# Performance work log

Hardware: AMD Instinct MI355X
Metric: run time of the kernel (lower is better)

Reference implementation:

```python
import jax, jax.numpy as jnp
import numpy as np

B, S, H, NL, DF, VF = 8, 2048, 8, 128, 64, 64
NF, HS = 1280, 33
FEAT = NF + HS
NLAYERS = 2
MAXLAP = 0.001


def setup_inputs() -> dict:
    key = jax.random.key(0)
    ks = jax.random.split(key, 11)
    u = lambda k, shape: jax.random.uniform(k, shape, jnp.float32, -0.01, 0.01)
    return {
        "latent_outputs": jax.random.normal(ks[0], (B, S, HS), jnp.float32),
        "masks": (jax.random.uniform(ks[1], (B, S, 1)) > 0.05).astype(jnp.float32),
        "x_embeds": jax.random.normal(ks[2], (B, S, NF), jnp.float32),
        "pos_embed": jax.random.normal(ks[3], (B, S, DF), jnp.float32),
        "collect_classes": u(ks[4], (1, VF * H, HS)),
        "query_linear": u(ks[5], (NLAYERS, 1, H, FEAT + 1, DF)),
        "key_linear": u(ks[6], (NLAYERS, 1, 1, FEAT + 1, DF)),
        "value_linear": u(ks[7], (NLAYERS, 1, H, FEAT + 1, VF)),
        "project_original": u(ks[8], (NLAYERS, 1, 1, FEAT + 1, VF)),
        "aggregation_params": u(ks[9], (NLAYERS, 1, H, 1, 1)),
        "collect_feats": u(ks[10], (NLAYERS - 1, VF * H, FEAT)),
    }


def _iterative_inv(mat, n_iter=6):
    I = jnp.eye(mat.shape[-1], dtype=mat.dtype)
    key = mat
    value = (1.0 / jnp.max(jnp.sum(key, axis=-2))) * jnp.swapaxes(key, -1, -2)
    for _ in range(n_iter):
        kv = key @ value
        value = 0.25 * value @ (13 * I - kv @ (15 * I - kv @ (7 * I - kv)))
    return value


def _compute_accum(values, masks, qw, kw, vw, agg):
    # values: [B,1,S,FEAT]; qw/vw: [1,H,FEAT+1,*], kw: [1,1,FEAT+1,DF]
    # NOTE: bias is the second-to-last row (as in the torch source, [..., -2:-1, :]).
    Eq = values @ qw[..., :-1, :] + qw[..., -2:-1, :]  # [B,H,S,DF]
    Ek = values @ kw[..., :-1, :] + kw[..., -2:-1, :]  # [B,1,S,DF]
    Ev = values @ vw[..., :-1, :] + vw[..., -2:-1, :]  # [B,H,S,VF]
    pos = jnp.arange(S)
    rel = jnp.abs(pos[None, None, None, :] - pos[None, None, :, None]).astype(values.dtype)
    sigmas = jnp.abs(agg) + MAXLAP          # [1,H,1,1]
    pos_mask = -sigmas * rel                # [1,H,S,S] Laplace position penalty
    scale = DF ** 0.25
    Eq = Eq / scale
    Ek = Ek / scale
    seg = S // NL
    q_land = Eq.reshape(Eq.shape[0], Eq.shape[1], NL, seg, DF).mean(-2)  # [B,H,NL,DF]
    k_land = Ek.reshape(Ek.shape[0], Ek.shape[1], NL, seg, DF).mean(-2)  # [B,1,NL,DF]
    pos_sel = pos_mask.reshape(1, H, NL, seg, S).mean(3)                 # [1,H,NL,S]
    kernel_1 = jax.nn.softmax(Eq @ jnp.swapaxes(k_land, -1, -2)
                              + jnp.swapaxes(pos_sel, -1, -2), axis=-1)  # [B,H,S,NL]
    pos_sel2 = pos_sel.reshape(1, H, NL, NL, seg).mean(-1)               # [1,H,NL,NL]
    kernel_2 = jax.nn.softmax(q_land @ jnp.swapaxes(k_land, -1, -2) + pos_sel2, axis=-1)
    scores = q_land @ jnp.swapaxes(Ek, -1, -2)                            # [B,H,NL,S]
    attn_mask = jnp.swapaxes(jnp.where(masks[:, None] == 0, -1e6, 0.0), -1, -2)  # [B,1,1,S]
    kernel_3 = jax.nn.softmax(scores + attn_mask + pos_sel, axis=-1)      # [B,H,NL,S]
    probs = kernel_1 @ _iterative_inv(kernel_2)                           # [B,H,S,NL]
    return probs @ (kernel_3 @ Ev)                                        # [B,H,S,VF]


def reference(latent_outputs, masks, x_embeds, pos_embed, collect_classes,
              query_linear, key_linear, value_linear, project_original,
              aggregation_params, collect_feats):
    cl = jax.nn.softmax(latent_outputs, axis=-1) * masks
    orig = jnp.concatenate([x_embeds, cl], axis=-1)[:, None]  # [B,1,S,FEAT]
    va = orig
    for layer in range(NLAYERS):
        va = _compute_accum(va, masks, query_linear[layer], key_linear[layer],
                            value_linear[layer], aggregation_params[layer])
        pw = project_original[layer, ..., :-1, :]
        pb = project_original[layer, ..., -2:-1, :]
        va = va + (orig @ pw + pb) / NLAYERS            # [B,H,S,VF]
        va = jnp.transpose(va, (0, 2, 1, 3)).reshape(B, S, H * VF)
        cw = collect_feats[layer] if layer < NLAYERS - 1 else collect_classes
        va = (va @ cw)[:, None]
    return va[:, 0] * masks  # [B,S,HS]
```

## Files before the change

### kernel.cpp

```cpp
#include <hip/hip_runtime.h>
#include <math.h>


namespace {

constexpr int B = 8, S = 2048, H = 8, NL = 128, DF = 64, VF = 64;
constexpr int NF = 1280, HS = 33, FEAT = 1313, FEATP = 1314;
constexpr int SEG = 16, HV = H * VF;
constexpr int KSF = 1344;
constexpr int NSPL = 4;
constexpr long ROWS = (long)B * S;
constexpr float INV_SCALE = 0.35355339059327373f;

typedef _Float16 f16;
typedef _Float16 f16x8 __attribute__((ext_vector_type(8)));
typedef _Float16 f16x4 __attribute__((ext_vector_type(4)));
typedef float f32x4 __attribute__((ext_vector_type(4)));

__global__ __launch_bounds__(256) void k_cl(
    const float* __restrict__ lat, const float* __restrict__ masks,
    float* __restrict__ cl)
{
  long row = (long)blockIdx.x * 4 + (threadIdx.x >> 6);
  int l = threadIdx.x & 63;
  float v = (l < HS) ? lat[row * HS + l] : -INFINITY;
  float m = v;
  #pragma unroll
  for (int o = 32; o; o >>= 1) m = fmaxf(m, __shfl_xor(m, o));
  float e = (l < HS) ? expf(v - m) : 0.f;
  float s = e;
  #pragma unroll
  for (int o = 32; o; o >>= 1) s += __shfl_xor(s, o);
  if (l < HS) cl[row * HS + l] = e / s * masks[row];
}

__global__ __launch_bounds__(256) void k_cvta(
    const float* __restrict__ xemb, const float* __restrict__ cl,
    f16* __restrict__ dst)
{
  long idx = (long)blockIdx.x * 256 + threadIdx.x;
  long row = idx / 168;
  int c = (int)(idx - row * 168);
  int t = c >> 3, cs = c & 7;
  int k0 = t * 64 + cs * 8;
  f16x8 v;
  if (t < 20) {
    float4 a = *(const float4*)&xemb[row * NF + k0];
    float4 b = *(const float4*)&xemb[row * NF + k0 + 4];
    v[0] = (f16)a.x; v[1] = (f16)a.y; v[2] = (f16)a.z; v[3] = (f16)a.w;
    v[4] = (f16)b.x; v[5] = (f16)b.y; v[6] = (f16)b.z; v[7] = (f16)b.w;
  } else {
    #pragma unroll
    for (int i = 0; i < 8; ++i) {
      int k = k0 + i;
      float f = 0.f;
      if (k < NF) f = xemb[row * NF + k];
      else if (k < FEAT) f = cl[row * HS + (k - NF)];
      v[i] = (f16)f;
    }
  }
  int cd = cs ^ ((int)row & 7);
  *(f16x8*)&dst[row * KSF + t * 64 + cd * 8] = v;
}

__global__ __launch_bounds__(256) void k_cvtw6(
    const float* __restrict__ qlin, const float* __restrict__ klin,
    const float* __restrict__ vlin, const float* __restrict__ plin,
    const float* __restrict__ cfeat, const float* __restrict__ ccls,
    f16* __restrict__ WQt, f16* __restrict__ WKt, f16* __restrict__ WVt,
    f16* __restrict__ WPt, f16* __restrict__ WCFt, f16* __restrict__ WCCt)
{
  constexpr long s1 = 172032, s2 = 193536, s3 = 365568, s4 = 387072,
                 s5 = 473088, s6 = 477184;
  long idx = (long)blockIdx.x * 256 + threadIdx.x;
  if (idx >= s6) return;
  const float* src; f16* dst; int K, N, Npad, KS; long srcZ, rel;
  if (idx < s1)      { src = qlin;  dst = WQt;  K = FEAT; N = 64;  Npad = 64;  KS = KSF; srcZ = (long)FEATP * 64; rel = idx; }
  else if (idx < s2) { src = klin;  dst = WKt;  K = FEAT; N = 64;  Npad = 64;  KS = KSF; srcZ = (long)FEATP * 64; rel = idx - s1; }
  else if (idx < s3) { src = vlin;  dst = WVt;  K = FEAT; N = 64;  Npad = 64;  KS = KSF; srcZ = (long)FEATP * 64; rel = idx - s2; }
  else if (idx < s4) { src = plin;  dst = WPt;  K = FEAT; N = 64;  Npad = 64;  KS = KSF; srcZ = (long)FEATP * 64; rel = idx - s3; }
  else if (idx < s5) { src = cfeat; dst = WCFt; K = 512;  N = FEAT; Npad = KSF; KS = 512; srcZ = 0; rel = idx - s4; }
  else               { src = ccls;  dst = WCCt; K = 512;  N = HS;  Npad = 64;  KS = 512; srcZ = 0; rel = idx - s5; }
  long cpz = (long)Npad * (KS >> 3);
  long z = rel / cpz;
  long rem = rel - z * cpz;
  int n = (int)(rem / (KS >> 3));
  int c = (int)(rem - (long)n * (KS >> 3));
  int t = c >> 3, cs = c & 7;
  int cd = cs ^ (n & 7);
  int k0 = t * 64 + cd * 8;
  const float* sp = src + z * srcZ;
  f16x8 v;
  #pragma unroll
  for (int i = 0; i < 8; ++i) {
    int k = k0 + i;
    v[i] = (f16)((k < K && n < N) ? sp[(long)k * N + n] : 0.f);
  }
  *(f16x8*)&dst[rel * 8] = v;
}

__global__ __launch_bounds__(256, 2) void k_mgemm(
    const f16* __restrict__ A, long aZOff, int aDiv,
    const f16* __restrict__ Wt, long wZOff, int wMod,
    int KT, int mode,
    float* __restrict__ C, long cZOff, int ldC,
    const float* __restrict__ biasBase, long biasZOff, float scale,
    f16* __restrict__ outA, int NR, const float* __restrict__ mask)
{
  const long KS = (long)KT * 64;
  int z = blockIdx.z;
  const f16* Ap = A + (long)(z / aDiv) * aZOff;
  const f16* Wp = Wt + (long)(z % wMod) * wZOff;
  long m0 = (long)blockIdx.x * 256;
  int n0 = blockIdx.y * 64;
  constexpr int BOFF = 256 * 64;
  __shared__ f16 lds[2][(256 + 64) * 64];
  int tid = threadIdx.x;
  int wv = tid >> 6, l = tid & 63;

  const f16* aW = Ap + (m0 + wv * 64 + (l >> 3)) * KS + (l & 7) * 8;
  const f16* bW = Wp + ((long)(n0 + wv * 16 + (l >> 3))) * KS + (l & 7) * 8;

  f32x4 acc[4][4];
  #pragma unroll
  for (int i = 0; i < 4; ++i)
    #pragma unroll
    for (int j = 0; j < 4; ++j) acc[i][j] = (f32x4){0.f, 0.f, 0.f, 0.f};

  auto stage = [&](int buf, int t) {
    f16* la = &lds[buf][(wv * 64) * 64];
    const f16* ga = aW + (long)t * 64;
// ... 69 lines not shown
      int coll = ni * 16 + lcn;
      int col = n0 + coll;
      bool ok = col < NR;
      #pragma unroll
      for (int mi = 0; mi < 4; ++mi) {
        int rowl = wv * 64 + mi * 16 + lr;
        #pragma unroll
        for (int r = 0; r < 4; ++r) {
          float v = ok ? acc[mi][ni][r] * scale : 0.f;
          st[(rowl + r) * 64 + coll] = (f16)v;
        }
      }
    }
    __syncthreads();
    int tt = n0 >> 6;
    for (int c = tid; c < 2048; c += 256) {
      int row = c >> 3, cd = c & 7;
      long grow = m0 + row;
      int r7 = (int)grow & 7;
      f16x8 v = *(const f16x8*)&st[row * 64 + cd * 8];
      *(f16x8*)&outA[grow * KSF + tt * 64 + ((cd ^ r7) << 3)] = v;
    }
  }
}

__global__ __launch_bounds__(256, 2) void k_qve(
    const f16* __restrict__ Aact, const f16* __restrict__ Aorig,
    const f16* __restrict__ WQl, const f16* __restrict__ WVl,
    const f16* __restrict__ wk, const f16* __restrict__ wp,
    const float* __restrict__ bqBase, const float* __restrict__ bvBase,
    const float* __restrict__ bk, const float* __restrict__ bp,
    f16* __restrict__ Eq16, f16* __restrict__ Ev16, f16* __restrict__ Ek16,
    float* __restrict__ projb,
    float* __restrict__ qland, f16* __restrict__ qland16,
    float* __restrict__ kland, f16* __restrict__ kland16)
{
  constexpr int KT = 21;
  __shared__ __align__(16) f16 shbuf[2 * 256 * 64];
  int bid = blockIdx.x;
  int tid = threadIdx.x;
  int wv = tid >> 6, l = tid & 63;
  int l15 = l & 15, lc = l >> 4, lx = l & 7;
  int lr = (l >> 4) * 4;
  int lcn = l & 15;

  if (bid < 1024) {
    constexpr int BOFF = 128 * 64;
    int z = bid >> 4;
    int h = z & 7;
    const f16* Ap = Aact + (long)(z >> 3) * S * KSF;
    const f16* wqp = WQl + (long)h * 64 * KSF;
    const f16* wvp = WVl + (long)h * 64 * KSF;
    const float* bq = bqBase + (long)h * FEATP * 64;
    const float* bv = bvBase + (long)h * FEATP * 64;
    long m0 = (long)(bid & 15) * 128;

    const f16* aW = Ap + (m0 + wv * 32 + (l >> 3)) * KSF + (l & 7) * 8;

    f32x4 acc[2][8];
    #pragma unroll
    for (int i = 0; i < 2; ++i)
      #pragma unroll
      for (int j = 0; j < 8; ++j) acc[i][j] = (f32x4){0.f, 0.f, 0.f, 0.f};

    auto stage = [&](int buf, int t) {
      f16* la = &shbuf[buf * 16384 + (wv * 32) * 64];
      const f16* ga = aW + (long)t * 64;
      #pragma unroll
// ... 47 lines not shown
        }
      __syncthreads();
    }

    f16* st = &shbuf[0];
    #pragma unroll
    for (int ni = 0; ni < 8; ++ni) {
      int col = ni * 16 + l15;
      float bvv = (col < 64) ? bq[col] : bv[col - 64];
      float scl = (col < 64) ? INV_SCALE : 1.f;
      #pragma unroll
      for (int mi = 0; mi < 2; ++mi) {
        int rowl = wv * 32 + mi * 16 + lr;
        #pragma unroll
        for (int r = 0; r < 4; ++r)
          st[(rowl + r) * 128 + col] = (f16)((acc[mi][ni][r] + bvv) * scl);
      }
    }
    __syncthreads();
    f16* oq = Eq16 + (long)z * S * 64;
    f16* ov = Ev16 + (long)z * S * 64;
    for (int c = tid; c < 1024; c += 256) {
      int rw = c >> 3, cc = c & 7;
      *(f16x8*)&oq[(m0 + rw) * 64 + cc * 8] = *(const f16x8*)&st[rw * 128 + cc * 8];
      *(f16x8*)&ov[(m0 + rw) * 64 + cc * 8] = *(const f16x8*)&st[rw * 128 + 64 + cc * 8];
    }
    for (int c = tid; c < 512; c += 256) {
      int lm = c >> 6, d = c & 63;
      float s = 0.f;
      #pragma unroll
      for (int i = 0; i < SEG; ++i) s += (float)st[(lm * SEG + i) * 128 + d];
      float v = s * (1.f / SEG);
      long li = (long)z * NL + (m0 >> 4) + lm;
      qland[li * 64 + d] = v;
      qland16[li * 64 + d] = (f16)v;
    }
  } else {
    constexpr int BOFF = 128 * 64;
    int rel = bid - 1024;
    int zz2 = rel >> 4;
    int prob = zz2 >> 3, b = zz2 & 7;
    const f16* Ap = (prob ? Aorig : Aact) + (long)b * S * KSF;
    const f16* Wp = prob ? wp : wk;
    long m0 = (long)(rel & 15) * 128;

    const f16* aW = Ap + (m0 + wv * 32 + (l >> 3)) * KSF + (l & 7) * 8;
    const f16* bW = Wp + ((long)(wv * 16 + (l >> 3))) * KSF + (l & 7) * 8;

    f32x4 acc[2][4];
    #pragma unroll
    for (int i = 0; i < 2; ++i)
      #pragma unroll
      for (int j = 0; j < 4; ++j) acc[i][j] = (f32x4){0.f, 0.f, 0.f, 0.f};

    auto stage = [&](int buf, int t) {
      f16* la = &shbuf[buf * 12288 + (wv * 32) * 64];
      const f16* ga = aW + (long)t * 64;
      #pragma unroll
      for (int j = 0; j < 4; ++j)
        __builtin_amdgcn_global_load_lds(
            (const __attribute__((address_space(1))) void*)(ga + (long)j * 8 * KSF),
            (__attribute__((address_space(3))) void*)(la + j * 512), 16, 0, 0);
      f16* lb = &shbuf[buf * 12288 + BOFF + (wv * 16) * 64];
      const f16* gb = bW + (long)t * 64;
      #pragma unroll
      for (int j = 0; j < 2; ++j)
        __builtin_amdgcn_global_load_lds(
// ... 31 lines not shown
          acc[mi][ni] = __builtin_amdgcn_mfma_f32_16x16x32_f16(af[mi][1], bf[ni][1], acc[mi][ni], 0, 0, 0);
        }
      __syncthreads();
    }

    if (prob == 0) {
      f16* st = &shbuf[0];
      #pragma unroll
      for (int ni = 0; ni < 4; ++ni) {
        int col = ni * 16 + lcn;
        float bv = bk[col];
        #pragma unroll
        for (int mi = 0; mi < 2; ++mi) {
          int rowl = wv * 32 + mi * 16 + lr;
          #pragma unroll
          for (int r = 0; r < 4; ++r)
            st[(rowl + r) * 64 + col] = (f16)((acc[mi][ni][r] + bv) * INV_SCALE);
        }
      }
      __syncthreads();
      f16* o16 = Ek16 + (long)b * S * 64;
      for (int c = tid; c < 1024; c += 256) {
        int row = c >> 3, cc = c & 7;
        f16x8 v = *(const f16x8*)&st[row * 64 + cc * 8];
        *(f16x8*)&o16[(m0 + row) * 64 + cc * 8] = v;
      }
      for (int c = tid; c < 512; c += 256) {
        int lm = c >> 6, d = c & 63;
        float s = 0.f;
        #pragma unroll
        for (int i = 0; i < SEG; ++i) s += (float)st[(lm * SEG + i) * 64 + d];
        float v = s * (1.f / SEG);
        long li = (long)b * NL + (m0 >> 4) + lm;
        kland[li * 64 + d] = v;
        kland16[li * 64 + d] = (f16)v;
      }
    } else {
      float* Cp = projb + (long)b * S * 64;
      #pragma unroll
      for (int ni = 0; ni < 4; ++ni) {
        int col = ni * 16 + lcn;
        float bv = bp[col];
        #pragma unroll
        for (int mi = 0; mi < 2; ++mi) {
          long row = m0 + wv * 32 + mi * 16 + lr;
          #pragma unroll
          for (int r = 0; r < 4; ++r)
            Cp[(row + r) * 64 + col] = (acc[mi][ni][r] + bv) * 0.5f;
        }
      }
    }
  }
}

__global__ __launch_bounds__(256) void k_kernel2(
    const float* __restrict__ qland, const float* __restrict__ kland,
    const float* __restrict__ aggL, f16* __restrict__ k2h,
    float* __restrict__ colmax)
{
  int z = blockIdx.x; int b = z / H; int h = z % H;
  float sigma = fabsf(aggL[h]) + 0.001f;
  __shared__ float qs[NL][68];
  __shared__ float ks[NL][68];
  __shared__ float lg[NL][NL + 1];
  int tid = threadIdx.x;
  for (int idx = tid; idx < NL * DF; idx += 256) {
    int r = idx >> 6, d = idx & 63;
    qs[r][d] = qland[((long)z * NL + r) * DF + d];
    ks[r][d] = kland[((long)b * NL + r) * DF + d];
  }
  __syncthreads();
  int r = tid >> 1, half = tid & 1;
  float lmax = -INFINITY;
  for (int c = 0; c < 64; c++) {
    int m = half * 64 + c;
    float s = 0.f;
    #pragma unroll
    for (int d = 0; d < DF; d += 4) {
      float4 q = *(const float4*)&qs[r][d];
      float4 k4 = *(const float4*)&ks[m][d];
      s += q.x * k4.x + q.y * k4.y + q.z * k4.z + q.w * k4.w;
    }
    float dd = fabsf((float)(r - m));
    s += -sigma * ((r == m) ? 5.3125f : 16.f * dd);
    lg[r][m] = s;
    lmax = fmaxf(lmax, s);
  }
  lmax = fmaxf(lmax, __shfl_xor(lmax, 1));
  float lsum = 0.f;
  for (int c = 0; c < 64; c++) {
    int m = half * 64 + c;
    float e = expf(lg[r][m] - lmax);
    lg[r][m] = e; lsum += e;
  }
  lsum += __shfl_xor(lsum, 1);
  float inv = 1.f / lsum;
  for (int c = 0; c < 64; c++) {
    int m = half * 64 + c;
    float p = lg[r][m] * inv;
    lg[r][m] = p;
    k2h[((long)z * NL + r) * NL + m] = (f16)p;
  }
  __syncthreads();
  float myc = 0.f;
  if (tid < NL) {
    for (int rr = 0; rr < NL; rr++) myc += lg[rr][tid];
  }
  float wm = myc;
  #pragma unroll
  for (int o = 32; o; o >>= 1) wm = fmaxf(wm, __shfl_xor(wm, o));
  __shared__ float wred[4];
  if ((tid & 63) == 0) wred[tid >> 6] = wm;
  __syncthreads();
  if (tid == 0)
    colmax[z] = fmaxf(fmaxf(wred[0], wred[1]), fmaxf(wred[2], wred[3]));
}

__global__ __launch_bounds__(256, 2) void k_kernel3(
    const f16* __restrict__ qland16, const f16* __restrict__ Ek16,
    const f16* __restrict__ Ev16, const float* __restrict__ aggL,
    const float* __restrict__ masks,
    float* __restrict__ partU, float* __restrict__ partML)
{
  __shared__ __align__(16) f16 Qs[64 * 64];
  __shared__ __align__(16) f16 Ks[128 * 64];
  __shared__ __align__(16) f16 Vt[64 * 128];
  __shared__ __align__(16) f16 Pb[4 * 16 * 128];
  __shared__ float Ms[128];
  int id = blockIdx.x;
  int chunk = id & (NSPL - 1);
  int z2 = id >> 2;
  int z = z2 >> 1, half = z2 & 1;
  int b = z >> 3, h = z & 7;
  int q0 = half * 64;
  int tid = threadIdx.x;
  int w = tid >> 6, l = tid & 63;
  float sigma = fabsf(aggL[h]) + 0.001f;
  float cpos = -sigma * (1.f / 16.f);

  for (int c = tid; c < 64 * 8; c += 256) {
    int q = c >> 3, kc = c & 7;
    f16x8 v = *(const f16x8*)&qland16[((long)z * NL + q0 + q) * 64 + kc * 8];
    *(f16x8*)&Qs[q * 64 + ((kc ^ (q & 7)) << 3)] = v;
  }

  f16* Pw = &Pb[w * 16 * 128];
  int l15 = l & 15, lg4 = l >> 4, l7 = l & 7;
  f32x4 Oa[4];
  #pragma unroll
  for (int i = 0; i < 4; ++i) Oa[i] = (f32x4){0.f, 0.f, 0.f, 0.f};
  float mrun[4] = {-INFINITY, -INFINITY, -INFINITY, -INFINITY};
  float lrun[4] = {0.f, 0.f, 0.f, 0.f};

  int t0beg = chunk * (S / 128 / NSPL), t0end = t0beg + S / 128 / NSPL;
  for (int t0 = t0beg; t0 < t0end; ++t0) {
    __syncthreads();
    for (int c = tid; c < 1024; c += 256) {
      int k = c >> 3, kc = c & 7;
      f16x8 v = *(const f16x8*)&Ek16[((long)b * S + t0 * 128 + k) * 64 + kc * 8];
      *(f16x8*)&Ks[k * 64 + ((kc ^ (k & 7)) << 3)] = v;
    }
    for (int c = tid; c < 1024; c += 256) {
      int k = c & 127, dc = c >> 7;
      f16x8 v = *(const f16x8*)&Ev16[((long)z * S + t0 * 128 + k) * 64 + dc * 8];
      int kc = k >> 3, ki = k & 7;
      #pragma unroll
      for (int j = 0; j < 8; ++j) {
        int d = dc * 8 + j;
        Vt[d * 128 + ((kc ^ (d & 7)) << 3) + ki] = v[j];
      }
    }
    if (tid < 128)
      Ms[tid] = (masks[(long)b * S + t0 * 128 + tid] == 0.f) ? -1e6f : 0.f;
    __syncthreads();

    f16x8 af[2];
    #pragma unroll
    for (int kh = 0; kh < 2; ++kh)
      af[kh] = *(const f16x8*)&Qs[(w * 16 + l15) * 64 + (((kh * 4 + lg4) ^ l7) << 3)];
    f32x4 sc[8];
    #pragma unroll
    for (int ct = 0; ct < 8; ++ct) {
      int n = ct * 16 + l15;
      f16x8 b0 = *(const f16x8*)&Ks[n * 64 + (((lg4) ^ (n & 7)) << 3)];
      f16x8 b1 = *(const f16x8*)&Ks[n * 64 + (((4 + lg4) ^ (n & 7)) << 3)];
      f32x4 zz = (f32x4){0.f, 0.f, 0.f, 0.f};
      zz = __builtin_amdgcn_mfma_f32_16x16x32_f16(af[0], b0, zz, 0, 0, 0);
      sc[ct] = __builtin_amdgcn_mfma_f32_16x16x32_f16(af[1], b1, zz, 0, 0, 0);
    }
    float tmax[4] = {-INFINITY, -INFINITY, -INFINITY, -INFINITY};
    #pragma unroll
    for (int ct = 0; ct < 8; ++ct) {
      float mk = Ms[ct * 16 + l15];
      int key = t0 * 128 + ct * 16 + l15;
      #pragma unroll
      for (int r = 0; r < 4; ++r) {
        int qg = q0 + w * 16 + lg4 * 4 + r;
        float a = (float)(key - 16 * qg);
        float ac = fminf(fmaxf(a, 0.f), 15.f);
        float dd = fabsf(a - ac);
        float sum = ac * ac - 15.f * ac + 120.f + 16.f * dd;
        float s = sc[ct][r] + cpos * sum + mk;
        sc[ct][r] = s;
        tmax[r] = fmaxf(tmax[r], s);
      }
    }
    #pragma unroll
    for (int r = 0; r < 4; ++r) {
      #pragma unroll
      for (int o = 1; o < 16; o <<= 1)
        tmax[r] = fmaxf(tmax[r], __shfl_xor(tmax[r], o));
    }
    float fr[4], lsum[4];
    #pragma unroll
    for (int r = 0; r < 4; ++r) {
      float mnew = fmaxf(mrun[r], tmax[r]);
      fr[r] = expf(mrun[r] - mnew);
      mrun[r] = mnew;
      lsum[r] = 0.f;
    }
    #pragma unroll
    for (int ct = 0; ct < 8; ++ct) {
      #pragma unroll
      for (int r = 0; r < 4; ++r) {
        float p = expf(sc[ct][r] - mrun[r]);
        sc[ct][r] = p;
        lsum[r] += p;
      }
    }
    #pragma unroll
    for (int r = 0; r < 4; ++r) {
      #pragma unroll
      for (int o = 1; o < 16; o <<= 1)
        lsum[r] += __shfl_xor(lsum[r], o);
      lrun[r] = lrun[r] * fr[r] + lsum[r];
    }
    f32x4 fv = (f32x4){fr[0], fr[1], fr[2], fr[3]};
    #pragma unroll
    for (int dt = 0; dt < 4; ++dt) Oa[dt] *= fv;
    #pragma unroll
    for (int ct = 0; ct < 8; ++ct) {
      int kc = ct * 2 + (l15 >> 3);
      int ki = l15 & 7;
      #pragma unroll
      for (int r = 0; r < 4; ++r) {
        int row = lg4 * 4 + r;
        Pw[row * 128 + ((kc ^ (row & 7)) << 3) + ki] = (f16)sc[ct][r];
      }
    }
    #pragma unroll
    for (int ks = 0; ks < 4; ++ks) {
      f16x8 pa = *(const f16x8*)&Pw[l15 * 128 + (((ks * 4 + lg4) ^ l7) << 3)];
      #pragma unroll
      for (int dt = 0; dt < 4; ++dt) {
        int n = dt * 16 + l15;
        f16x8 bv = *(const f16x8*)&Vt[n * 128 + (((ks * 4 + lg4) ^ (n & 7)) << 3)];
        Oa[dt] = __builtin_amdgcn_mfma_f32_16x16x32_f16(pa, bv, Oa[dt], 0, 0, 0);
      }
    }
  }
  #pragma unroll
  for (int r = 0; r < 4; ++r) {
    long qg = q0 + w * 16 + lg4 * 4 + r;
    long base = ((long)z * NL + qg) * NSPL + chunk;
    #pragma unroll
    for (int dt = 0; dt < 4; ++dt)
      partU[base * 64 + dt * 16 + l15] = Oa[dt][r];
    if (l15 == 0) {
      partML[base * 2] = mrun[r];
      partML[base * 2 + 1] = lrun[r];
    }
  }
}

__global__ __launch_bounds__(512) void k_inverse(
    const f16* __restrict__ k2h, const float* __restrict__ colmax,
    const float* __restrict__ partU, const float* __restrict__ partML,
    float* __restrict__ m2)
{
  __shared__ __align__(16) f16 bufA[128 * 128];
  __shared__ __align__(16) f16 bufB[128 * 128];
  __shared__ __align__(16) f16 Vt[128 * 128];
  __shared__ __align__(16) f16 Pt[128 * 128];
  int z = blockIdx.x;
  int tid = threadIdx.x;
  int w = tid >> 6, l = tid & 63;
  int l15 = l & 15, lg4 = l >> 4;
  int wr = (w >> 1) * 32, wc = (w & 1) * 64;

  float cv = colmax[l];
  #pragma unroll
  for (int o = 32; o; o >>= 1) cv = fmaxf(cv, __shfl_xor(cv, o));
  float recip = 1.f / cv;

  const f16* key = k2h + (long)z * NL * NL;
  auto swz = [](int r, int c) { return r * 128 + ((((c >> 3) ^ (r & 15))) << 3) + (c & 7); };

  for (int idx = tid; idx < 128 * 16; idx += 512) {
    int r = idx >> 4, c8 = (idx & 15) << 3;
    f16x8 kk = *(const f16x8*)&key[r * 128 + c8];
    f16x8 sv;
    #pragma unroll
    for (int j = 0; j < 8; ++j) sv[j] = (f16)(recip * (float)kk[j]);
    *(f16x8*)&Vt[swz(r, c8)] = sv;
// ... 248 lines not shown
  const float* masks = (const float*)d_in[1];
  const float* xemb  = (const float*)d_in[2];
  const float* ccls  = (const float*)d_in[4];
  const float* qlin  = (const float*)d_in[5];
  const float* klin  = (const float*)d_in[6];
  const float* vlin  = (const float*)d_in[7];
  const float* plin  = (const float*)d_in[8];
  const float* agg   = (const float*)d_in[9];
  const float* cfeat = (const float*)d_in[10];
  float* out = (float*)d_out;
  float* ws = (float*)d_ws;

  long off = 0;
  auto allocF = [&](long n) { float* p = ws + off; off += (n + 3) & ~3L; return p; };
  auto allocH = [&](long n) { f16* p = (f16*)(ws + off); off += ((n + 1) / 2 + 3) & ~3L; return p; };

  f16* origA = allocH(ROWS * KSF);
  f16* vbufA = allocH(ROWS * KSF);
  f16* merged = allocH(ROWS * (long)HV);
  f16* WQt = allocH(16L * 64 * KSF);
  f16* WKt = allocH(2L * 64 * KSF);
  f16* WVt = allocH(16L * 64 * KSF);
  f16* WPt = allocH(2L * 64 * KSF);
  f16* WCFt = allocH((long)KSF * 512);
  f16* WCCt = allocH(64L * 512);
  f16* Ek16 = allocH((long)B * S * 64);
  f16* Ev16 = allocH((long)B * H * S * 64);
  f16* Eq16 = allocH((long)B * H * S * 64);
  f16* qland16 = allocH((long)B * H * NL * DF);
  f16* kland16 = allocH((long)B * NL * DF);
  f16* k2h = allocH((long)B * H * NL * NL);
  float* cl     = allocF(ROWS * HS);
  float* projb  = allocF((long)B * S * VF);
  float* qland  = allocF((long)B * H * NL * DF);
  float* kland  = allocF((long)B * NL * DF);
  float* m2b    = allocF((long)B * H * NL * VF);
  float* colmax = allocF(64);
  float* partU  = allocF((long)B * H * NL * NSPL * 64);
  float* partML = allocF((long)B * H * NL * NSPL * 2);

  k_cl<<<(int)(ROWS / 4), 256, 0, stream>>>(lat, masks, cl);
  k_cvta<<<(int)(ROWS * 168 / 256), 256, 0, stream>>>(xemb, cl, origA);
  k_cvtw6<<<1864, 256, 0, stream>>>(qlin, klin, vlin, plin, cfeat, ccls,
      WQt, WKt, WVt, WPt, WCFt, WCCt);

  const f16* Aact = origA;
  for (int layer = 0; layer < 2; ++layer) {
    const f16* wq = WQt + (long)layer * 8 * 64 * KSF;
    const f16* wk = WKt + (long)layer * 64 * KSF;
    const f16* wvv = WVt + (long)layer * 8 * 64 * KSF;
    const f16* wp = WPt + (long)layer * 64 * KSF;
    const float* bq = qlin + (long)layer * 8 * FEATP * 64 + (long)(FEATP - 2) * 64;
    const float* bk = klin + (long)layer * FEATP * 64 + (long)(FEATP - 2) * 64;
    const float* bv = vlin + (long)layer * 8 * FEATP * 64 + (long)(FEATP - 2) * 64;
    const float* bp = plin + (long)layer * FEATP * 64 + (long)(FEATP - 2) * 64;
    const float* ag = agg + layer * H;

    k_qve<<<1280, 256, 0, stream>>>(Aact, origA, wq, wvv, wk, wp,
        bq, bv, bk, bp, Eq16, Ev16, Ek16, projb,
        qland, qland16, kland, kland16);

    k_kernel2<<<B * H, 256, 0, stream>>>(qland, kland, ag, k2h, colmax);
    k_kernel3<<<B * H * 2 * NSPL, 256, 0, stream>>>(qland16, Ek16, Ev16, ag, masks,
        partU, partML);
    k_inverse<<<B * H, 512, 0, stream>>>(k2h, colmax, partU, partML, m2b);
    k_k1attn<<<B * H * (S / 64), 256, 0, stream>>>(Eq16, kland16, ag, m2b, projb, merged);

    if (layer == 0) {
      dim3 gC(64, 21, 1);
      k_mgemm<<<gC, 256, 0, stream>>>(merged, 0, 1, WCFt, 0, 1, 8, 1,
          nullptr, 0, 0, nullptr, 0, 1.0f, vbufA, FEAT, nullptr);
      Aact = vbufA;
    } else {
      dim3 gO(64, 1, 1);
      k_mgemm<<<gO, 256, 0, stream>>>(merged, 0, 1, WCCt, 0, 1, 8, 2,
          out, 0, HS, nullptr, 0, 1.0f, nullptr, HS, masks);
    }
  }
  (void)in_sizes; (void)n_in; (void)out_size; (void)ws_size;
}
```

Before: 492.4 us.

## Merge prep kernels and fuse landmark kernel2/kernel3 into one MFMA launch

Merges the activation and weight fp16 conversion kernels into a single launch, and merges the landmark-softmax (kernel_2) and landmark-to-sequence attention (kernel_3) kernels into one launch split by block index. The kernel_2 path now uses fp16 MFMA on the fp16 landmark copies instead of fp32 scalar dot products, so the fp32 landmark buffers and their stores are removed. This cuts launch count and lets the small 64-block kernel_2 run concurrently with kernel_3. In exchange, kernel_2 scores are computed from fp16 inputs, which lowers precision ahead of the iterative inverse.

```diff
diff --git a/kernel.cpp b/kernel.cpp
--- a/kernel.cpp
+++ b/kernel.cpp
@@ -34,69 +34,70 @@
   if (l < HS) cl[row * HS + l] = e / s * masks[row];
 }
 
-__global__ __launch_bounds__(256) void k_cvta(
+__global__ __launch_bounds__(256) void k_prep(
     const float* __restrict__ xemb, const float* __restrict__ cl,
-    f16* __restrict__ dst)
-{
-  long idx = (long)blockIdx.x * 256 + threadIdx.x;
-  long row = idx / 168;
-  int c = (int)(idx - row * 168);
-  int t = c >> 3, cs = c & 7;
-  int k0 = t * 64 + cs * 8;
-  f16x8 v;
-  if (t < 20) {
-    float4 a = *(const float4*)&xemb[row * NF + k0];
-    float4 b = *(const float4*)&xemb[row * NF + k0 + 4];
-    v[0] = (f16)a.x; v[1] = (f16)a.y; v[2] = (f16)a.z; v[3] = (f16)a.w;
-    v[4] = (f16)b.x; v[5] = (f16)b.y; v[6] = (f16)b.z; v[7] = (f16)b.w;
-  } else {
-    #pragma unroll
-    for (int i = 0; i < 8; ++i) {
-      int k = k0 + i;
-      float f = 0.f;
-      if (k < NF) f = xemb[row * NF + k];
-      else if (k < FEAT) f = cl[row * HS + (k - NF)];
-      v[i] = (f16)f;
-    }
-  }
-  int cd = cs ^ ((int)row & 7);
-  *(f16x8*)&dst[row * KSF + t * 64 + cd * 8] = v;
-}
-
-__global__ __launch_bounds__(256) void k_cvtw6(
     const float* __restrict__ qlin, const float* __restrict__ klin,
     const float* __restrict__ vlin, const float* __restrict__ plin,
     const float* __restrict__ cfeat, const float* __restrict__ ccls,
+    f16* __restrict__ origA,
     f16* __restrict__ WQt, f16* __restrict__ WKt, f16* __restrict__ WVt,
     f16* __restrict__ WPt, f16* __restrict__ WCFt, f16* __restrict__ WCCt)
 {
-  constexpr long s1 = 172032, s2 = 193536, s3 = 365568, s4 = 387072,
-                 s5 = 473088, s6 = 477184;
-  long idx = (long)blockIdx.x * 256 + threadIdx.x;
-  if (idx >= s6) return;
-  const float* src; f16* dst; int K, N, Npad, KS; long srcZ, rel;
-  if (idx < s1)      { src = qlin;  dst = WQt;  K = FEAT; N = 64;  Npad = 64;  KS = KSF; srcZ = (long)FEATP * 64; rel = idx; }
-  else if (idx < s2) { src = klin;  dst = WKt;  K = FEAT; N = 64;  Npad = 64;  KS = KSF; srcZ = (long)FEATP * 64; rel = idx - s1; }
-  else if (idx < s3) { src = vlin;  dst = WVt;  K = FEAT; N = 64;  Npad = 64;  KS = KSF; srcZ = (long)FEATP * 64; rel = idx - s2; }
-  else if (idx < s4) { src = plin;  dst = WPt;  K = FEAT; N = 64;  Npad = 64;  KS = KSF; srcZ = (long)FEATP * 64; rel = idx - s3; }
-  else if (idx < s5) { src = cfeat; dst = WCFt; K = 512;  N = FEAT; Npad = KSF; KS = 512; srcZ = 0; rel = idx - s4; }
-  else               { src = ccls;  dst = WCCt; K = 512;  N = HS;  Npad = 64;  KS = 512; srcZ = 0; rel = idx - s5; }
-  long cpz = (long)Npad * (KS >> 3);
-  long z = rel / cpz;
-  long rem = rel - z * cpz;
-  int n = (int)(rem / (KS >> 3));
-  int c = (int)(rem - (long)n * (KS >> 3));
-  int t = c >> 3, cs = c & 7;
-  int cd = cs ^ (n & 7);
-  int k0 = t * 64 + cd * 8;
-  const float* sp = src + z * srcZ;
-  f16x8 v;
-  #pragma unroll
-  for (int i = 0; i < 8; ++i) {
-    int k = k0 + i;
-    v[i] = (f16)((k < K && n < N) ? sp[(long)k * N + n] : 0.f);
-  }
-  *(f16x8*)&dst[rel * 8] = v;
+  long bid = blockIdx.x;
+  int tid = threadIdx.x;
+  if (bid < 10752) {
+    long idx = bid * 256 + tid;
+    long row = idx / 168;
+    int c = (int)(idx - row * 168);
+    int t = c >> 3, cs = c & 7;
+    int k0 = t * 64 + cs * 8;
+    f16x8 v;
+    if (t < 20) {
+      float4 a = *(const float4*)&xemb[row * NF + k0];
+      float4 b = *(const float4*)&xemb[row * NF + k0 + 4];
+      v[0] = (f16)a.x; v[1] = (f16)a.y; v[2] = (f16)a.z; v[3] = (f16)a.w;
+      v[4] = (f16)b.x; v[5] = (f16)b.y; v[6] = (f16)b.z; v[7] = (f16)b.w;
+    } else {
+      #pragma unroll
+      for (int i = 0; i < 8; ++i) {
+        int k = k0 + i;
+        float f = 0.f;
+        if (k < NF) f = xemb[row * NF + k];
+        else if (k < FEAT) f = cl[row * HS + (k - NF)];
+        v[i] = (f16)f;
+      }
+    }
+    int cd = cs ^ ((int)row & 7);
+    *(f16x8*)&origA[row * KSF + t * 64 + cd * 8] = v;
+  } else {
+    constexpr long s1 = 172032, s2 = 193536, s3 = 365568, s4 = 387072,
+                   s5 = 473088, s6 = 477184;
+    long idx = (bid - 10752) * 256 + tid;
+    if (idx >= s6) return;
+    const float* src; f16* dst; int K, N, Npad, KS; long srcZ, rel;
+    if (idx < s1)      { src = qlin;  dst = WQt;  K = FEAT; N = 64;  Npad = 64;  KS = KSF; srcZ = (long)FEATP * 64; rel = idx; }
+    else if (idx < s2) { src = klin;  dst = WKt;  K = FEAT; N = 64;  Npad = 64;  KS = KSF; srcZ = (long)FEATP * 64; rel = idx - s1; }
+    else if (idx < s3) { src = vlin;  dst = WVt;  K = FEAT; N = 64;  Npad = 64;  KS = KSF; srcZ = (long)FEATP * 64; rel = idx - s2; }
+    else if (idx < s4) { src = plin;  dst = WPt;  K = FEAT; N = 64;  Npad = 64;  KS = KSF; srcZ = (long)FEATP * 64; rel = idx - s3; }
+    else if (idx < s5) { src = cfeat; dst = WCFt; K = 512;  N = FEAT; Npad = KSF; KS = 512; srcZ = 0; rel = idx - s4; }
+    else               { src = ccls;  dst = WCCt; K = 512;  N = HS;  Npad = 64;  KS = 512; srcZ = 0; rel = idx - s5; }
+    long cpz = (long)Npad * (KS >> 3);
+    long z = rel / cpz;
+    long rem = rel - z * cpz;
+    int n = (int)(rem / (KS >> 3));
+    int c = (int)(rem - (long)n * (KS >> 3));
+    int t = c >> 3, cs = c & 7;
+    int cd = cs ^ (n & 7);
+    int k0 = t * 64 + cd * 8;
+    const float* sp = src + z * srcZ;
+    f16x8 v;
+    #pragma unroll
+    for (int i = 0; i < 8; ++i) {
+      int k = k0 + i;
+      v[i] = (f16)((k < K && n < N) ? sp[(long)k * N + n] : 0.f);
+    }
+    *(f16x8*)&dst[rel * 8] = v;
+  }
 }
 
 __global__ __launch_bounds__(256, 2) void k_mgemm(
@@ -232,8 +233,7 @@
     const float* __restrict__ bk, const float* __restrict__ bp,
     f16* __restrict__ Eq16, f16* __restrict__ Ev16, f16* __restrict__ Ek16,
     float* __restrict__ projb,
-    float* __restrict__ qland, f16* __restrict__ qland16,
-    float* __restrict__ kland, f16* __restrict__ kland16)
+    f16* __restrict__ qland16, f16* __restrict__ kland16)
 {
   constexpr int KT = 21;
   __shared__ __align__(16) f16 shbuf[2 * 256 * 64];
@@ -347,7 +347,6 @@
       for (int i = 0; i < SEG; ++i) s += (float)st[(lm * SEG + i) * 128 + d];
       float v = s * (1.f / SEG);
       long li = (long)z * NL + (m0 >> 4) + lm;
-      qland[li * 64 + d] = v;
       qland16[li * 64 + d] = (f16)v;
     }
   } else {
@@ -445,7 +444,6 @@
         for (int i = 0; i < SEG; ++i) s += (float)st[(lm * SEG + i) * 64 + d];
         float v = s * (1.f / SEG);
         long li = (long)b * NL + (m0 >> 4) + lm;
-        kland[li * 64 + d] = v;
         kland16[li * 64 + d] = (f16)v;
       }
     } else {
@@ -466,223 +464,274 @@
   }
 }
 
-__global__ __launch_bounds__(256) void k_kernel2(
-    const float* __restrict__ qland, const float* __restrict__ kland,
-    const float* __restrict__ aggL, f16* __restrict__ k2h,
-    float* __restrict__ colmax)
+__global__ __launch_bounds__(256, 2) void k_land(
+    const f16* __restrict__ qland16, const f16* __restrict__ kland16,
+    const f16* __restrict__ Ek16, const f16* __restrict__ Ev16,
+    const float* __restrict__ aggL, const float* __restrict__ masks,
+    float* __restrict__ partU, float* __restrict__ partML,
+    f16* __restrict__ k2h, float* __restrict__ colmax)
 {
-  int z = blockIdx.x; int b = z / H; int h = z % H;
-  float sigma = fabsf(aggL[h]) + 0.001f;
-  __shared__ float qs[NL][68];
-  __shared__ float ks[NL][68];
-  __shared__ float lg[NL][NL + 1];
-  int tid = threadIdx.x;
-  for (int idx = tid; idx < NL * DF; idx += 256) {
-    int r = idx >> 6, d = idx & 63;
-    qs[r][d] = qland[((long)z * NL + r) * DF + d];
-    ks[r][d] = kland[((long)b * NL + r) * DF + d];
-  }
-  __syncthreads();
-  int r = tid >> 1, half = tid & 1;
-  float lmax = -INFINITY;
-  for (int c = 0; c < 64; c++) {
-    int m = half * 64 + c;
-    float s = 0.f;
-    #pragma unroll
-    for (int d = 0; d < DF; d += 4) {
-      float4 q = *(const float4*)&qs[r][d];
-      float4 k4 = *(const float4*)&ks[m][d];
-      s += q.x * k4.x + q.y * k4.y + q.z * k4.z + q.w * k4.w;
-    }
-    float dd = fabsf((float)(r - m));
-    s += -sigma * ((r == m) ? 5.3125f : 16.f * dd);
-    lg[r][m] = s;
-    lmax = fmaxf(lmax, s);
-  }
-  lmax = fmaxf(lmax, __shfl_xor(lmax, 1));
-  float lsum = 0.f;
-  for (int c = 0; c < 64; c++) {
-    int m = half * 64 + c;
-    float e = expf(lg[r][m] - lmax);
-    lg[r][m] = e; lsum += e;
-  }
-  lsum += __shfl_xor(lsum, 1);
-  float inv = 1.f / lsum;
-  for (int c = 0; c < 64; c++) {
-    int m = half * 64 + c;
-    float p = lg[r][m] * inv;
-    lg[r][m] = p;
-    k2h[((long)z * NL + r) * NL + m] = (f16)p;
-  }
-  __syncthreads();
-  float myc = 0.f;
-  if (tid < NL) {
-    for (int rr = 0; rr < NL; rr++) myc += lg[rr][tid];
-  }
-  float wm = myc;
-  #pragma unroll
-  for (int o = 32; o; o >>= 1) wm = fmaxf(wm, __shfl_xor(wm, o));
-  __shared__ float wred[4];
-  if ((tid & 63) == 0) wred[tid >> 6] = wm;
-  __syncthreads();
-  if (tid == 0)
-    colmax[z] = fmaxf(fmaxf(wred[0], wred[1]), fmaxf(wred[2], wred[3]));
-}
-
-__global__ __launch_bounds__(256, 2) void k_kernel3(
-    const f16* __restrict__ qland16, const f16* __restrict__ Ek16,
-    const f16* __restrict__ Ev16, const float* __restrict__ aggL,
-    const float* __restrict__ masks,
-    float* __restrict__ partU, float* __restrict__ partML)
-{
-  __shared__ __align__(16) f16 Qs[64 * 64];
-  __shared__ __align__(16) f16 Ks[128 * 64];
-  __shared__ __align__(16) f16 Vt[64 * 128];
-  __shared__ __align__(16) f16 Pb[4 * 16 * 128];
-  __shared__ float Ms[128];
-  int id = blockIdx.x;
-  int chunk = id & (NSPL - 1);
-  int z2 = id >> 2;
-  int z = z2 >> 1, half = z2 & 1;
-  int b = z >> 3, h = z & 7;
-  int q0 = half * 64;
+  __shared__ __align__(16) unsigned char smem[57856];
+  int bid = blockIdx.x;
   int tid = threadIdx.x;
   int w = tid >> 6, l = tid & 63;
-  float sigma = fabsf(aggL[h]) + 0.001f;
-  float cpos = -sigma * (1.f / 16.f);
-
-  for (int c = tid; c < 64 * 8; c += 256) {
-    int q = c >> 3, kc = c & 7;
-    f16x8 v = *(const f16x8*)&qland16[((long)z * NL + q0 + q) * 64 + kc * 8];
-    *(f16x8*)&Qs[q * 64 + ((kc ^ (q & 7)) << 3)] = v;
-  }
-
-  f16* Pw = &Pb[w * 16 * 128];
   int l15 = l & 15, lg4 = l >> 4, l7 = l & 7;
-  f32x4 Oa[4];
-  #pragma unroll
-  for (int i = 0; i < 4; ++i) Oa[i] = (f32x4){0.f, 0.f, 0.f, 0.f};
-  float mrun[4] = {-INFINITY, -INFINITY, -INFINITY, -INFINITY};
-  float lrun[4] = {0.f, 0.f, 0.f, 0.f};
-
-  int t0beg = chunk * (S / 128 / NSPL), t0end = t0beg + S / 128 / NSPL;
-  for (int t0 = t0beg; t0 < t0end; ++t0) {
+
+  if (bid < 512) {
+    f16* Qs = (f16*)smem;
+    f16* Ks = (f16*)(smem + 8192);
+    f16* Vt = (f16*)(smem + 24576);
+    f16* Pb = (f16*)(smem + 40960);
+    float* Ms = (float*)(smem + 57344);
+    int chunk = bid & (NSPL - 1);
+    int z2 = bid >> 2;
+    int z = z2 >> 1, half = z2 & 1;
+    int b = z >> 3, h = z & 7;
+    int q0 = half * 64;
+    float sigma = fabsf(aggL[h]) + 0.001f;
+    float cpos = -sigma * (1.f / 16.f);
+
+    for (int c = tid; c < 64 * 8; c += 256) {
+      int q = c >> 3, kc = c & 7;
+      f16x8 v = *(const f16x8*)&qland16[((long)z * NL + q0 + q) * 64 + kc * 8];
+      *(f16x8*)&Qs[q * 64 + ((kc ^ (q & 7)) << 3)] = v;
+    }
+
+    f16* Pw = &Pb[w * 16 * 128];
+    f32x4 Oa[4];
+    #pragma unroll
+    for (int i = 0; i < 4; ++i) Oa[i] = (f32x4){0.f, 0.f, 0.f, 0.f};
+    float mrun[4] = {-INFINITY, -INFINITY, -INFINITY, -INFINITY};
+    float lrun[4] = {0.f, 0.f, 0.f, 0.f};
+
+    int t0beg = chunk * (S / 128 / NSPL), t0end = t0beg + S / 128 / NSPL;
+    for (int t0 = t0beg; t0 < t0end; ++t0) {
+      __syncthreads();
+      for (int c = tid; c < 1024; c += 256) {
+        int k = c >> 3, kc = c & 7;
+        f16x8 v = *(const f16x8*)&Ek16[((long)b * S + t0 * 128 + k) * 64 + kc * 8];
+        *(f16x8*)&Ks[k * 64 + ((kc ^ (k & 7)) << 3)] = v;
+      }
+      for (int c = tid; c < 1024; c += 256) {
+        int k = c & 127, dc = c >> 7;
+        f16x8 v = *(const f16x8*)&Ev16[((long)z * S + t0 * 128 + k) * 64 + dc * 8];
+        int kc = k >> 3, ki = k & 7;
+        #pragma unroll
+        for (int j = 0; j < 8; ++j) {
+          int d = dc * 8 + j;
+          Vt[d * 128 + ((kc ^ (d & 7)) << 3) + ki] = v[j];
+        }
+      }
+      if (tid < 128)
+        Ms[tid] = (masks[(long)b * S + t0 * 128 + tid] == 0.f) ? -1e6f : 0.f;
+      __syncthreads();
+
+      f16x8 af[2];
+      #pragma unroll
+      for (int kh = 0; kh < 2; ++kh)
+        af[kh] = *(const f16x8*)&Qs[(w * 16 + l15) * 64 + (((kh * 4 + lg4) ^ l7) << 3)];
+      f32x4 sc[8];
+      #pragma unroll
+      for (int ct = 0; ct < 8; ++ct) {
+        int n = ct * 16 + l15;
+        f16x8 b0 = *(const f16x8*)&Ks[n * 64 + (((lg4) ^ (n & 7)) << 3)];
+        f16x8 b1 = *(const f16x8*)&Ks[n * 64 + (((4 + lg4) ^ (n & 7)) << 3)];
+        f32x4 zz = (f32x4){0.f, 0.f, 0.f, 0.f};
+        zz = __builtin_amdgcn_mfma_f32_16x16x32_f16(af[0], b0, zz, 0, 0, 0);
+        sc[ct] = __builtin_amdgcn_mfma_f32_16x16x32_f16(af[1], b1, zz, 0, 0, 0);
+      }
+      float tmax[4] = {-INFINITY, -INFINITY, -INFINITY, -INFINITY};
+      #pragma unroll
+      for (int ct = 0; ct < 8; ++ct) {
+        float mk = Ms[ct * 16 + l15];
+        int key = t0 * 128 + ct * 16 + l15;
+        #pragma unroll
+        for (int r = 0; r < 4; ++r) {
+          int qg = q0 + w * 16 + lg4 * 4 + r;
+          float a = (float)(key - 16 * qg);
+          float ac = fminf(fmaxf(a, 0.f), 15.f);
+          float dd = fabsf(a - ac);
+          float sum = ac * ac - 15.f * ac + 120.f + 16.f * dd;
+          float s = sc[ct][r] + cpos * sum + mk;
+          sc[ct][r] = s;
+          tmax[r] = fmaxf(tmax[r], s);
+        }
+      }
+      #pragma unroll
+      for (int r = 0; r < 4; ++r) {
+        #pragma unroll
+        for (int o = 1; o < 16; o <<= 1)
+          tmax[r] = fmaxf(tmax[r], __shfl_xor(tmax[r], o));
+      }
+      float fr[4], lsum[4];
+      #pragma unroll
+      for (int r = 0; r < 4; ++r) {
+        float mnew = fmaxf(mrun[r], tmax[r]);
+        fr[r] = expf(mrun[r] - mnew);
+        mrun[r] = mnew;
+        lsum[r] = 0.f;
+      }
+      #pragma unroll
+      for (int ct = 0; ct < 8; ++ct) {
+        #pragma unroll
+        for (int r = 0; r < 4; ++r) {
+          float p = expf(sc[ct][r] - mrun[r]);
+          sc[ct][r] = p;
+          lsum[r] += p;
+        }
+      }
+      #pragma unroll
+      for (int r = 0; r < 4; ++r) {
+        #pragma unroll
+        for (int o = 1; o < 16; o <<= 1)
+          lsum[r] += __shfl_xor(lsum[r], o);
+        lrun[r] = lrun[r] * fr[r] + lsum[r];
+      }
+      f32x4 fv = (f32x4){fr[0], fr[1], fr[2], fr[3]};
+      #pragma unroll
+      for (int dt = 0; dt < 4; ++dt) Oa[dt] *= fv;
+      #pragma unroll
+      for (int ct = 0; ct < 8; ++ct) {
+        int kc = ct * 2 + (l15 >> 3);
+        int ki = l15 & 7;
+        #pragma unroll
+        for (int r = 0; r < 4; ++r) {
+          int row = lg4 * 4 + r;
+          Pw[row * 128 + ((kc ^ (row & 7)) << 3) + ki] = (f16)sc[ct][r];
+        }
+      }
+      #pragma unroll
+      for (int ks = 0; ks < 4; ++ks) {
+        f16x8 pa = *(const f16x8*)&Pw[l15 * 128 + (((ks * 4 + lg4) ^ l7) << 3)];
+        #pragma unroll
+        for (int dt = 0; dt < 4; ++dt) {
+          int n = dt * 16 + l15;
+          f16x8 bv = *(const f16x8*)&Vt[n * 128 + (((ks * 4 + lg4) ^ (n & 7)) << 3)];
+          Oa[dt] = __builtin_amdgcn_mfma_f32_16x16x32_f16(pa, bv, Oa[dt], 0, 0, 0);
+        }
+      }
+    }
+    #pragma unroll
+    for (int r = 0; r < 4; ++r) {
+      long qg = q0 + w * 16 + lg4 * 4 + r;
+      long base = ((long)z * NL + qg) * NSPL + chunk;
+      #pragma unroll
+      for (int dt = 0; dt < 4; ++dt)
+        partU[base * 64 + dt * 16 + l15] = Oa[dt][r];
+      if (l15 == 0) {
+        partML[base * 2] = mrun[r];
+        partML[base * 2 + 1] = lrun[r];
+      }
+    }
+  } else {
+    f16* Qs2 = (f16*)smem;
+    f16* Ks2 = (f16*)(smem + 16384);
+    float* colpart = (float*)(smem + 32768);
+    int z = bid - 512;
+    int b2 = z >> 3, h2 = z & 7;
+    float sigma = fabsf(aggL[h2]) + 0.001f;
+    for (int c = tid; c < 1024; c += 256) {
+      int q = c >> 3, kc = c & 7;
+      f16x8 v = *(const f16x8*)&qland16[((long)z * NL + q) * 64 + kc * 8];
+      *(f16x8*)&Qs2[q * 64 + ((kc ^ (q & 7)) << 3)] = v;
+      f16x8 u = *(const f16x8*)&kland16[((long)b2 * NL + q) * 64 + kc * 8];
+      *(f16x8*)&Ks2[q * 64 + ((kc ^ (q & 7)) << 3)] = u;
+    }
     __syncthreads();
-    for (int c = tid; c < 1024; c += 256) {
-      int k = c >> 3, kc = c & 7;
-      f16x8 v = *(const f16x8*)&Ek16[((long)b * S + t0 * 128 + k) * 64 + kc * 8];
-      *(f16x8*)&Ks[k * 64 + ((kc ^ (k & 7)) << 3)] = v;
-    }
-    for (int c = tid; c < 1024; c += 256) {
-      int k = c & 127, dc = c >> 7;
-      f16x8 v = *(const f16x8*)&Ev16[((long)z * S + t0 * 128 + k) * 64 + dc * 8];
-      int kc = k >> 3, ki = k & 7;
-      #pragma unroll
-      for (int j = 0; j < 8; ++j) {
-        int d = dc * 8 + j;
-        Vt[d * 128 + ((kc ^ (d & 7)) << 3) + ki] = v[j];
-      }
-    }
-    if (tid < 128)
-      Ms[tid] = (masks[(long)b * S + t0 * 128 + tid] == 0.f) ? -1e6f : 0.f;
+    f32x4 acc[2][8];
+    #pragma unroll
+    for (int i = 0; i < 2; ++i)
+      #pragma unroll
+      for (int j = 0; j < 8; ++j) acc[i][j] = (f32x4){0.f, 0.f, 0.f, 0.f};
+    f16x8 af[2][2];
+    #pragma unroll
+    for (int mi = 0; mi < 2; ++mi)
+      #pragma unroll
+      for (int kh = 0; kh < 2; ++kh)
+        af[mi][kh] = *(const f16x8*)&Qs2[(w * 32 + mi * 16 + l15) * 64 + (((kh * 4 + lg4) ^ l7) << 3)];
+    #pragma unroll
+    for (int ni = 0; ni < 8; ++ni) {
+      int n = ni * 16 + l15;
+      f16x8 b0 = *(const f16x8*)&Ks2[n * 64 + ((lg4 ^ (n & 7)) << 3)];
+      f16x8 b1 = *(const f16x8*)&Ks2[n * 64 + (((4 + lg4) ^ (n & 7)) << 3)];
+      #pragma unroll
+      for (int mi = 0; mi < 2; ++mi) {
+        acc[mi][ni] = __builtin_amdgcn_mfma_f32_16x16x32_f16(af[mi][0], b0, acc[mi][ni], 0, 0, 0);
+        acc[mi][ni] = __builtin_amdgcn_mfma_f32_16x16x32_f16(af[mi][1], b1, acc[mi][ni], 0, 0, 0);
+      }
+    }
+    float colp[8];
+    #pragma unroll
+    for (int ni = 0; ni < 8; ++ni) colp[ni] = 0.f;
+    f16* o2 = k2h + (long)z * NL * NL;
+    #pragma unroll
+    for (int mi = 0; mi < 2; ++mi) {
+      float tmax[4] = {-INFINITY, -INFINITY, -INFINITY, -INFINITY};
+      #pragma unroll
+      for (int ni = 0; ni < 8; ++ni) {
+        int m = ni * 16 + l15;
+        #pragma unroll
+        for (int r = 0; r < 4; ++r) {
+          int row = w * 32 + mi * 16 + lg4 * 4 + r;
+          float dd = fabsf((float)(row - m));
+          float s = acc[mi][ni][r] - sigma * ((row == m) ? 5.3125f : 16.f * dd);
+          acc[mi][ni][r] = s;
+          tmax[r] = fmaxf(tmax[r], s);
+        }
+      }
+      #pragma unroll
+      for (int r = 0; r < 4; ++r) {
+        #pragma unroll
+        for (int o = 1; o < 16; o <<= 1)
+          tmax[r] = fmaxf(tmax[r], __shfl_xor(tmax[r], o));
+      }
+      float lsum2[4] = {0.f, 0.f, 0.f, 0.f};
+      #pragma unroll
+      for (int ni = 0; ni < 8; ++ni)
+        #pragma unroll
+        for (int r = 0; r < 4; ++r) {
+          float e = expf(acc[mi][ni][r] - tmax[r]);
+          acc[mi][ni][r] = e;
+          lsum2[r] += e;
+        }
+      #pragma unroll
+      for (int r = 0; r < 4; ++r) {
+        #pragma unroll
+        for (int o = 1; o < 16; o <<= 1)
+          lsum2[r] += __shfl_xor(lsum2[r], o);
+        lsum2[r] = 1.f / lsum2[r];
+      }
+      #pragma unroll
+      for (int ni = 0; ni < 8; ++ni) {
+        int m = ni * 16 + l15;
+        #pragma unroll
+        for (int r = 0; r < 4; ++r) {
+          float p = acc[mi][ni][r] * lsum2[r];
+          o2[(long)(w * 32 + mi * 16 + lg4 * 4 + r) * NL + m] = (f16)p;
+          colp[ni] += p;
+        }
+      }
+    }
+    #pragma unroll
+    for (int ni = 0; ni < 8; ++ni) {
+      colp[ni] += __shfl_xor(colp[ni], 16);
+      colp[ni] += __shfl_xor(colp[ni], 32);
+    }
+    if (lg4 == 0) {
+      #pragma unroll
+      for (int ni = 0; ni < 8; ++ni)
+        colpart[w * 128 + ni * 16 + l15] = colp[ni];
+    }
     __syncthreads();
-
-    f16x8 af[2];
-    #pragma unroll
-    for (int kh = 0; kh < 2; ++kh)
-      af[kh] = *(const f16x8*)&Qs[(w * 16 + l15) * 64 + (((kh * 4 + lg4) ^ l7) << 3)];
-    f32x4 sc[8];
-    #pragma unroll
-    for (int ct = 0; ct < 8; ++ct) {
-      int n = ct * 16 + l15;
-      f16x8 b0 = *(const f16x8*)&Ks[n * 64 + (((lg4) ^ (n & 7)) << 3)];
-      f16x8 b1 = *(const f16x8*)&Ks[n * 64 + (((4 + lg4) ^ (n & 7)) << 3)];
-      f32x4 zz = (f32x4){0.f, 0.f, 0.f, 0.f};
-      zz = __builtin_amdgcn_mfma_f32_16x16x32_f16(af[0], b0, zz, 0, 0, 0);
-      sc[ct] = __builtin_amdgcn_mfma_f32_16x16x32_f16(af[1], b1, zz, 0, 0, 0);
-    }
-    float tmax[4] = {-INFINITY, -INFINITY, -INFINITY, -INFINITY};
-    #pragma unroll
-    for (int ct = 0; ct < 8; ++ct) {
-      float mk = Ms[ct * 16 + l15];
-      int key = t0 * 128 + ct * 16 + l15;
-      #pragma unroll
-      for (int r = 0; r < 4; ++r) {
-        int qg = q0 + w * 16 + lg4 * 4 + r;
-        float a = (float)(key - 16 * qg);
-        float ac = fminf(fmaxf(a, 0.f), 15.f);
-        float dd = fabsf(a - ac);
-        float sum = ac * ac - 15.f * ac + 120.f + 16.f * dd;
-        float s = sc[ct][r] + cpos * sum + mk;
-        sc[ct][r] = s;
-        tmax[r] = fmaxf(tmax[r], s);
-      }
-    }
-    #pragma unroll
-    for (int r = 0; r < 4; ++r) {
-      #pragma unroll
-      for (int o = 1; o < 16; o <<= 1)
-        tmax[r] = fmaxf(tmax[r], __shfl_xor(tmax[r], o));
-    }
-    float fr[4], lsum[4];
-    #pragma unroll
-    for (int r = 0; r < 4; ++r) {
-      float mnew = fmaxf(mrun[r], tmax[r]);
-      fr[r] = expf(mrun[r] - mnew);
-      mrun[r] = mnew;
-      lsum[r] = 0.f;
-    }
-    #pragma unroll
-    for (int ct = 0; ct < 8; ++ct) {
-      #pragma unroll
-      for (int r = 0; r < 4; ++r) {
-        float p = expf(sc[ct][r] - mrun[r]);
-        sc[ct][r] = p;
-        lsum[r] += p;
-      }
-    }
-    #pragma unroll
-    for (int r = 0; r < 4; ++r) {
-      #pragma unroll
-      for (int o = 1; o < 16; o <<= 1)
-        lsum[r] += __shfl_xor(lsum[r], o);
-      lrun[r] = lrun[r] * fr[r] + lsum[r];
-    }
-    f32x4 fv = (f32x4){fr[0], fr[1], fr[2], fr[3]};
-    #pragma unroll
-    for (int dt = 0; dt < 4; ++dt) Oa[dt] *= fv;
-    #pragma unroll
-    for (int ct = 0; ct < 8; ++ct) {
-      int kc = ct * 2 + (l15 >> 3);
-      int ki = l15 & 7;
-      #pragma unroll
-      for (int r = 0; r < 4; ++r) {
-        int row = lg4 * 4 + r;
-        Pw[row * 128 + ((kc ^ (row & 7)) << 3) + ki] = (f16)sc[ct][r];
-      }
-    }
-    #pragma unroll
-    for (int ks = 0; ks < 4; ++ks) {
-      f16x8 pa = *(const f16x8*)&Pw[l15 * 128 + (((ks * 4 + lg4) ^ l7) << 3)];
-      #pragma unroll
-      for (int dt = 0; dt < 4; ++dt) {
-        int n = dt * 16 + l15;
-        f16x8 bv = *(const f16x8*)&Vt[n * 128 + (((ks * 4 + lg4) ^ (n & 7)) << 3)];
-        Oa[dt] = __builtin_amdgcn_mfma_f32_16x16x32_f16(pa, bv, Oa[dt], 0, 0, 0);
-      }
-    }
-  }
-  #pragma unroll
-  for (int r = 0; r < 4; ++r) {
-    long qg = q0 + w * 16 + lg4 * 4 + r;
-    long base = ((long)z * NL + qg) * NSPL + chunk;
-    #pragma unroll
-    for (int dt = 0; dt < 4; ++dt)
-      partU[base * 64 + dt * 16 + l15] = Oa[dt][r];
-    if (l15 == 0) {
-      partML[base * 2] = mrun[r];
-      partML[base * 2 + 1] = lrun[r];
-    }
+    if (tid < 128) {
+      float cs = colpart[tid] + colpart[128 + tid] + colpart[256 + tid] + colpart[384 + tid];
+      float wm = cs;
+      #pragma unroll
+      for (int o = 32; o; o >>= 1) wm = fmaxf(wm, __shfl_xor(wm, o));
+      if ((tid & 63) == 0) colpart[512 + (tid >> 6)] = wm;
+    }
+    __syncthreads();
+    if (tid == 0) colmax[z] = fmaxf(colpart[512], colpart[513]);
   }
 }
 
@@ -997,17 +1046,14 @@
   f16* k2h = allocH((long)B * H * NL * NL);
   float* cl     = allocF(ROWS * HS);
   float* projb  = allocF((long)B * S * VF);
-  float* qland  = allocF((long)B * H * NL * DF);
-  float* kland  = allocF((long)B * NL * DF);
   float* m2b    = allocF((long)B * H * NL * VF);
   float* colmax = allocF(64);
   float* partU  = allocF((long)B * H * NL * NSPL * 64);
   float* partML = allocF((long)B * H * NL * NSPL * 2);
 
   k_cl<<<(int)(ROWS / 4), 256, 0, stream>>>(lat, masks, cl);
-  k_cvta<<<(int)(ROWS * 168 / 256), 256, 0, stream>>>(xemb, cl, origA);
-  k_cvtw6<<<1864, 256, 0, stream>>>(qlin, klin, vlin, plin, cfeat, ccls,
-      WQt, WKt, WVt, WPt, WCFt, WCCt);
+  k_prep<<<10752 + 1864, 256, 0, stream>>>(xemb, cl, qlin, klin, vlin, plin,
+      cfeat, ccls, origA, WQt, WKt, WVt, WPt, WCFt, WCCt);
 
   const f16* Aact = origA;
   for (int layer = 0; layer < 2; ++layer) {
@@ -1022,12 +1068,10 @@
     const float* ag = agg + layer * H;
 
     k_qve<<<1280, 256, 0, stream>>>(Aact, origA, wq, wvv, wk, wp,
-        bq, bv, bk, bp, Eq16, Ev16, Ek16, projb,
-        qland, qland16, kland, kland16);
-
-    k_kernel2<<<B * H, 256, 0, stream>>>(qland, kland, ag, k2h, colmax);
-    k_kernel3<<<B * H * 2 * NSPL, 256, 0, stream>>>(qland16, Ek16, Ev16, ag, masks,
-        partU, partML);
+        bq, bv, bk, bp, Eq16, Ev16, Ek16, projb, qland16, kland16);
+
+    k_land<<<576, 256, 0, stream>>>(qland16, kland16, Ek16, Ev16, ag, masks,
+        partU, partML, k2h, colmax);
     k_inverse<<<B * H, 512, 0, stream>>>(k2h, colmax, partU, partML, m2b);
     k_k1attn<<<B * H * (S / 64), 256, 0, stream>>>(Eq16, kland16, ag, m2b, projb, merged);
 
```

Measured after the change: 438.9 us. -10.9%, faster.
